# Optimization experiments

Measured on AMD Instinct MI355X. Metric: run time of the kernel, lower is better.

Reference implementation:

```python
import jax, jax.numpy as jnp
import numpy as np

M1, M2, BS = 2000, 400, 8
AT = M1 + M2
E1, E2, E3 = 60000, 20000, 20000
H, F, NG, L, C = 64, 64, 50, 4, 4
CUTOFF = 10.0
LOG2 = 0.6931471805599453  # shift of ShiftedSoftplus


def _ssp(x):
    return jax.nn.softplus(x) - LOG2


def _smear(d):
    # GaussianSmearing(0, cutoff, NG)
    offset = jnp.linspace(0.0, CUTOFF, NG)
    coeff = -0.5 / (offset[1] - offset[0]) ** 2
    return jnp.exp(coeff * (d[:, None] - offset[None, :]) ** 2)  # [E, NG]


def _colored_mlp(attr, colors, w1, b1, w2, b2):
    # w1:[C,NG,F] b1:[C,F] w2:[C,F,F] b2:[C,F]; route each edge through its color's MLP
    out = jnp.zeros((attr.shape[0], w1.shape[-1]), attr.dtype)
    for c in range(C):  # fixed small color count
        h = _ssp(attr @ w1[c] + b1[c]) @ w2[c] + b2[c]
        out = out + jnp.where((colors == c)[:, None], h, jnp.zeros((), attr.dtype))
    return out


def _block(h, ei, ew, attr, col, p):
    # InteractionBlock: CFConv -> ssp -> linear
    mw1, mb1, mw2, mb2, cw1, cw2, cb2, bw, bb = p
    Ccut = 0.5 * (jnp.cos(ew * jnp.pi / CUTOFF) + 1.0)
    W = _colored_mlp(attr, col, mw1, mb1, mw2, mb2) * Ccut[:, None]  # [E,F]
    x = h @ cw1                                   # lin1 (no bias) [N,F]
    msg = x[ei[:, 0]] * W                         # gather x_j, modulate
    agg = jax.ops.segment_sum(msg, ei[:, 1], num_segments=h.shape[0])  # scatter-add
    x = agg @ cw2 + cb2                           # lin2
    return _ssp(x) @ bw + bb                      # act + block linear


def _batch_graph(ei, ew, col):
    # replicate per-structure edges across the batch with node offset b*AT
    offs = (jnp.arange(BS, dtype=ei.dtype) * AT)[:, None, None]
    ei_b = (ei[None] + offs).reshape(-1, 2)
    return ei_b, jnp.tile(ew, BS), jnp.tile(col, BS)


def _forward(sites, sites_p, e1, ew1, c1, e2, ew2, c2, e3, ew3, c3,
             emb_w, emb_p_w, mlp_w1, mlp_b1, mlp_w2, mlp_b2,
             conv_w1, conv_w2, conv_b2, blk_w, blk_b,
             out_w1, out_b1, out_w2, out_b2):
    h = jnp.concatenate([emb_w[sites], emb_p_w[sites_p]], axis=1).reshape(BS * AT, H)
    graphs = []
    for (ei, ew, col) in ((e1, ew1, c1), (e2, ew2, c2), (e3, ew3, c3)):
        ei_b, ew_b, col_b = _batch_graph(ei, ew, col)
        graphs.append((ei_b, ew_b, col_b, _smear(ew_b)))
    for l in range(L):
        delta = jnp.zeros_like(h)
        for g, (ei_b, ew_b, col_b, attr_b) in enumerate(graphs):
            p = (mlp_w1[l, g], mlp_b1[l, g], mlp_w2[l, g], mlp_b2[l, g],
                 conv_w1[l, g], conv_w2[l, g], conv_b2[l, g], blk_w[l, g], blk_b[l, g])
            delta = delta + _block(h, ei_b, ew_b, attr_b, col_b, p)
        h = h + delta
    hp = h.reshape(BS, AT, H)[:, M1:, :]   # mask selects pore nodes only
    o = hp @ out_w1 + out_b1               # NB: original has `h - self.act(h)` no-op, so no activation here
    o = o @ out_w2 + out_b2                # [BS, M2, 1]
    return o.sum(axis=1)                   # 'add' readout per batch -> [BS, 1]


def setup_inputs() -> dict:
    key = jax.random.key(0)
    ks = jax.random.split(key, 24)
    f = lambda i, shape, s=0.1: jax.random.normal(ks[i], shape, jnp.float32) * s
    sites = jax.random.randint(ks[0], (BS, M1), 0, 1, dtype=jnp.int32)
    sites_p = jax.random.randint(ks[1], (BS, M2), 0, 2, dtype=jnp.int32)
    e1 = jax.random.randint(ks[2], (E1, 2), 0, M1, dtype=jnp.int32)
    e2 = jnp.stack([jax.random.randint(ks[3], (E2,), 0, M1, dtype=jnp.int32),
                    jax.random.randint(ks[4], (E2,), M1, AT, dtype=jnp.int32)], 1)
    e3 = jnp.stack([jax.random.randint(ks[5], (E3,), M1, AT, dtype=jnp.int32),
                    jax.random.randint(ks[6], (E3,), 0, M1, dtype=jnp.int32)], 1)
    ew1 = jax.random.uniform(ks[7], (E1,), jnp.float32, 0.5, CUTOFF)
    ew2 = jax.random.uniform(ks[8], (E2,), jnp.float32, 0.5, CUTOFF)
    ew3 = jax.random.uniform(ks[9], (E3,), jnp.float32, 0.5, CUTOFF)
    c1 = jax.random.randint(ks[10], (E1,), 0, C, dtype=jnp.int32)
    c2 = jax.random.randint(ks[11], (E2,), 0, C, dtype=jnp.int32)
    c3 = jax.random.randint(ks[12], (E3,), 0, C, dtype=jnp.int32)
    return {
        'sites': sites, 'sites_p': sites_p,
        'edge_idx1': e1, 'edge_weight1': ew1, 'colors1': c1,
        'edge_idx2': e2, 'edge_weight2': ew2, 'colors2': c2,
        'edge_idx3': e3, 'edge_weight3': ew3, 'colors3': c3,
        'emb_w': f(13, (1, H), 1.0), 'emb_p_w': f(14, (2, H), 1.0),
        'mlp_w1': f(15, (L, 3, C, NG, F)), 'mlp_b1': jnp.zeros((L, 3, C, F), jnp.float32),
        'mlp_w2': f(16, (L, 3, C, F, F)), 'mlp_b2': jnp.zeros((L, 3, C, F), jnp.float32),
        'conv_w1': f(17, (L, 3, H, F)), 'conv_w2': f(18, (L, 3, F, H)),
        'conv_b2': jnp.zeros((L, 3, H), jnp.float32),
        'blk_w': f(19, (L, 3, H, H)), 'blk_b': jnp.zeros((L, 3, H), jnp.float32),
        'out_w1': f(20, (H, H // 2)), 'out_b1': jnp.zeros((H // 2,), jnp.float32),
        'out_w2': f(21, (H // 2, 1)), 'out_b2': jnp.zeros((1,), jnp.float32),
    }


def reference(sites, sites_p, edge_idx1, edge_weight1, colors1,
              edge_idx2, edge_weight2, colors2, edge_idx3, edge_weight3, colors3,
              emb_w, emb_p_w, mlp_w1, mlp_b1, mlp_w2, mlp_b2,
              conv_w1, conv_w2, conv_b2, blk_w, blk_b,
              out_w1, out_b1, out_w2, out_b2):
    return _forward(sites, sites_p, edge_idx1, edge_weight1, colors1,
                    edge_idx2, edge_weight2, colors2, edge_idx3, edge_weight3, colors3,
                    emb_w, emb_p_w, mlp_w1, mlp_b1, mlp_w2, mlp_b2,
                    conv_w1, conv_w2, conv_b2, blk_w, blk_b,
                    out_w1, out_b1, out_w2, out_b2)
```

## Files before the change

kernel.cpp:

```cpp
#include <hip/hip_runtime.h>
#include <math.h>

constexpr int M1 = 2000, M2 = 400, BS = 8;
constexpr int AT = M1 + M2;
constexpr int NN = BS * AT;
constexpr int E1 = 60000, E2 = 20000, E3 = 20000;
constexpr int ET = E1 + E2 + E3;
constexpr int H = 64, F = 64, NG = 50, L = 4, C = 4;
constexpr float CUTOFF = 10.0f;
constexpr float LOG2F_ = 0.6931471805599453f;

constexpr float SMEAR_STEP = 10.0f / 49.0f;
constexpr float SMEAR_COEFF = -12.005f;
constexpr float PI_OVER_CUT = 0.31415926535897932f;

constexpr int NBLK = (ET + 255) / 256;

constexpr int NT = 512;
constexpr float DSCALE = (float)(NT - 1) / CUTOFF;

constexpr int TILE_M = 32;
constexpr int MT = NN / TILE_M;

constexpr int NB0 = M1 / 4;
constexpr int NB1 = M2 / 4;
constexpr int NB2 = M1 / 4;
constexpr int NBTOT = NB0 + NB1 + NB2;

constexpr size_t O_HA    = 0;
constexpr size_t O_HB    = O_HA  + (size_t)NN * 64 * 4;
constexpr size_t O_XG    = O_HB  + (size_t)NN * 64 * 4;
constexpr size_t O_DG    = O_XG  + (size_t)3 * AT * 512 * 2;
constexpr size_t O_TAB2  = O_DG  + (size_t)3 * NN * 64 * 4;
constexpr size_t O_EDATA = O_TAB2 + (size_t)48 * NT * 64 * 8;
constexpr size_t O_INT   = O_EDATA + (size_t)ET * 16;
constexpr int I_DEG  = 0;
constexpr int I_CUR  = 7200;
constexpr int I_ZEND = 14400;
constexpr int I_BASE = 14400;
constexpr int I_PERM = 21616;

__device__ inline float sspf(float x) {
    return fmaxf(x, 0.0f) + log1pf(expf(-fabsf(x))) - LOG2F_;
}
__device__ inline float sspf_fast(float x) {
    float t = __expf(-fabsf(x));
    return fmaxf(x, 0.0f) + __logf(1.0f + t) - LOG2F_;
}

__device__ inline unsigned short bf16rn(float x) {
    unsigned int u = __float_as_uint(x);
    u = (u + 0x7FFFu + ((u >> 16) & 1u)) >> 16;
    return (unsigned short)u;
}

__device__ inline int graph_off(int g) { return g == 0 ? 0 : (g == 1 ? E1 : E1 + E2); }

__device__ inline void edge_decode(int idx, int& g, int& e,
                                   const int* ei1, const int* ei2, const int* ei3,
                                   const int* c1, const int* c2, const int* c3,
                                   const int*& ei, const int*& cl) {
    if (idx < E1)            { g = 0; e = idx;           ei = ei1; cl = c1; }
    else if (idx < E1 + E2)  { g = 1; e = idx - E1;      ei = ei2; cl = c2; }
    else                     { g = 2; e = idx - E1 - E2; ei = ei3; cl = c3; }
}

__global__ void k_init_h(const int* __restrict__ sites, const int* __restrict__ sites_p,
                         const float* __restrict__ emb_w, const float* __restrict__ emb_p_w,
                         float* __restrict__ h) {
    int idx = blockIdx.x * blockDim.x + threadIdx.x;
    if (idx >= NN * 64) return;
    int f = idx & 63;
    int n = idx >> 6;
    int b = n / AT;
    int i = n - b * AT;
    float v;
    if (i < M1) v = emb_w[sites[b * M1 + i] * H + f];
    else        v = emb_p_w[sites_p[b * M2 + (i - M1)] * H + f];
    h[idx] = v;
}

__global__ void k_count(const int* __restrict__ ei1, const int* __restrict__ ei2,
                        const int* __restrict__ ei3, const int* __restrict__ c1,
                        const int* __restrict__ c2, const int* __restrict__ c3,
                        int* __restrict__ deg) {
    int idx = blockIdx.x * blockDim.x + threadIdx.x;
    if (idx >= ET) return;
    int g, e; const int* ei; const int* cl;
    edge_decode(idx, g, e, ei1, ei2, ei3, c1, c2, c3, ei, cl);
    atomicAdd(&deg[g * AT + ei[2 * e + 1]], 1);
}

__global__ void k_scan(const int* __restrict__ deg, int* __restrict__ base) {
    const int T = 256, CH = 10;
    int t = threadIdx.x;
    __shared__ int lsum[T];
    int g = blockIdx.x;
    int loc[CH];
    int s = 0;
    #pragma unroll
    for (int i = 0; i < CH; i++) {
        int idx = t * CH + i;
        int v = (idx < AT) ? deg[g * AT + idx] : 0;
        loc[i] = s;
        s += v;
    }
    lsum[t] = s;
    __syncthreads();
    for (int off = 1; off < T; off <<= 1) {
        int v = 0;
        if (t >= off) v = lsum[t - off];
        __syncthreads();
        lsum[t] += v;
        __syncthreads();
    }
    int tb = lsum[t] - s;
    #pragma unroll
    for (int i = 0; i < CH; i++) {
        int idx = t * CH + i;
        if (idx < AT) base[g * (AT + 1) + idx] = tb + loc[i];
    }
    if (t == T - 1) base[g * (AT + 1) + AT] = lsum[T - 1];
}

__global__ void k_sort(const int* __restrict__ deg, int* __restrict__ perm) {
    __shared__ int hist[256];
    __shared__ int cur[256];
    int g = blockIdx.x, t = threadIdx.x;
    int off   = (g == 1) ? M1 : 0;
    int cnt   = (g == 1) ? M2 : M1;
    int pbase = (g == 0) ? 0 : ((g == 1) ? M1 : (M1 + M2));
    hist[t] = 0;
    __syncthreads();
    for (int i = t; i < cnt; i += 256)
        atomicAdd(&hist[min(deg[g * AT + off + i], 255)], 1);
    __syncthreads();
    if (t == 0) {
        int run = 0;
        for (int k = 0; k < 256; k++) { cur[k] = run; run += hist[k]; }
    }
    __syncthreads();
    for (int i = t; i < cnt; i += 256) {
        int pos = atomicAdd(&cur[min(deg[g * AT + off + i], 255)], 1);
        perm[pbase + pos] = off + i;
    }
}

__global__ void k_fill(const int* __restrict__ ei1, const int* __restrict__ ei2,
                       const int* __restrict__ ei3, const int* __restrict__ c1,
                       const int* __restrict__ c2, const int* __restrict__ c3,
                       const float* __restrict__ ew1, const float* __restrict__ ew2,
                       const float* __restrict__ ew3,
                       const int* __restrict__ base, int* __restrict__ cur,
                       int4* __restrict__ edata) {
    int idx = blockIdx.x * blockDim.x + threadIdx.x;
    if (idx >= ET) return;
    int g, e; const int* ei; const int* cl;
    edge_decode(idx, g, e, ei1, ei2, ei3, c1, c2, c3, ei, cl);
    const float* ew = (g == 0) ? ew1 : (g == 1 ? ew2 : ew3);
    int dst = ei[2 * e + 1];
    int src = ei[2 * e];
    int p = base[g * (AT + 1) + dst] + atomicAdd(&cur[g * AT + dst], 1);
    float t = ew[e] * DSCALE;
    int i0 = min((int)t, NT - 2);
    float fr = t - (float)i0;
    int cb = cl[e] * (L * NT) + i0;
    edata[graph_off(g) + p] = make_int4(src, cb, __float_as_int(fr), 0);
}

__global__ __launch_bounds__(256) void k_table(
    const float* __restrict__ mlp_w1, const float* __restrict__ mlp_b1,
    const float* __restrict__ mlp_w2, const float* __restrict__ mlp_b2,
    float* __restrict__ tab2) {
    const int lane = threadIdx.x & 63;
    int w = blockIdx.x * 4 + (threadIdx.x >> 6);
    int s = w >> 9;
    int p = w & (NT - 1);
    int l = s % L;
    int gc = s / L;
    int c = gc % C;
    int g = gc / C;
    float d = (float)p * (CUTOFF / (float)(NT - 1));

    size_t wb = (size_t)((l * 3 + g) * C + c);
    const float* w1 = mlp_w1 + wb * NG * F;
    const float* w2 = mlp_w2 + wb * F * F;
    float w1c[NG], w2c[F];
    #pragma unroll
    for (int k = 0; k < NG; k++) w1c[k] = w1[k * F + lane];
    #pragma unroll
    for (int k = 0; k < F; k++) w2c[k] = w2[k * F + lane];
    float b1c = mlp_b1[wb * F + lane];
    float b2c = mlp_b2[wb * F + lane];

    float dd = d - (float)lane * SMEAR_STEP;
    float av = (lane < NG) ? __expf(SMEAR_COEFF * dd * dd) : 0.0f;
    float acc = b1c;
    #pragma unroll
    for (int k = 0; k < NG; k++) acc = fmaf(__shfl(av, k), w1c[k], acc);
    float t = sspf_fast(acc);
    float acc2 = b2c;
    #pragma unroll
    for (int j = 0; j < F; j++) acc2 = fmaf(__shfl(t, j), w2c[j], acc2);
    float ccut = 0.5f * (__cosf(d * PI_OVER_CUT) + 1.0f);
    float val = acc2 * ccut;
    tab2[((size_t)s * NT + p) * 128 + lane * 2] = val;
    if (p > 0)
        tab2[((size_t)s * NT + (p - 1)) * 128 + lane * 2 + 1] = val;
}

__device__ inline void fma4(float acc[4], float a, const float4 b) {
    acc[0] = fmaf(a, b.x, acc[0]);
    acc[1] = fmaf(a, b.y, acc[1]);
    acc[2] = fmaf(a, b.z, acc[2]);
    acc[3] = fmaf(a, b.w, acc[3]);
}

__device__ inline void stage_A(const float* __restrict__ gA, float (*As)[68], int t) {
    #pragma unroll
    for (int i = 0; i < 2; i++) {
        int v = t + i * 256;
        int r = v >> 4, c4 = (v & 15) * 4;
        *(float4*)&As[r][c4] = *(const float4*)(gA + (size_t)r * 64 + c4);
    }
}
__device__ inline void stage_B(const float* __restrict__ gB, float (*Bs)[68], int t) {
    #pragma unroll
    for (int i = 0; i < 4; i++) {
        int v = t + i * 256;
        int r = v >> 4, c4 = (v & 15) * 4;
        *(float4*)&Bs[r][c4] = *(const float4*)(gB + (size_t)r * 64 + c4);
    }
}
__device__ inline void gemm_tile(const float (*As)[68], const float (*Bs)[68],
                                 int r0, int c0, float acc0[4], float acc1[4]) {
    #pragma unroll 4
    for (int k0 = 0; k0 < 64; k0 += 4) {
        float4 a0 = *(const float4*)&As[r0][k0];
        float4 a1 = *(const float4*)&As[r0 + 1][k0];
        float4 b0 = *(const float4*)&Bs[k0][c0];
        float4 b1 = *(const float4*)&Bs[k0 + 1][c0];
        float4 b2 = *(const float4*)&Bs[k0 + 2][c0];
        float4 b3 = *(const float4*)&Bs[k0 + 3][c0];
        fma4(acc0, a0.x, b0); fma4(acc0, a0.y, b1);
        fma4(acc0, a0.z, b2); fma4(acc0, a0.w, b3);
        fma4(acc1, a1.x, b0); fma4(acc1, a1.y, b1);
        fma4(acc1, a1.z, b2); fma4(acc1, a1.w, b3);
    }
}

__device__ inline void store_xg(unsigned short* __restrict__ xg, int g, int n,
                                int c0, const float acc[4]) {
    int b = n / AT;
    int i = n - b * AT;
    unsigned short* out = xg + (((size_t)g * AT + i) * 8 + b) * 64 + c0;
    ushort4 v;
    v.x = bf16rn(acc[0]);
    v.y = bf16rn(acc[1]);
    v.z = bf16rn(acc[2]);
    v.w = bf16rn(acc[3]);
    *(ushort4*)out = v;
}

__global__ __launch_bounds__(256) void k_lin1t(
    const float* __restrict__ h, const float* __restrict__ conv_w1,
    unsigned short* __restrict__ xg, int l) {
    __shared__ float As[TILE_M][68];
    __shared__ float Bs[64][68];
    int t = threadIdx.x;
    int g = blockIdx.x / MT;
    int tile = blockIdx.x - g * MT;
    stage_A(h + (size_t)tile * TILE_M * 64, As, t);
    stage_B(conv_w1 + (size_t)(l * 3 + g) * 64 * 64, Bs, t);
    __syncthreads();
    int cg = t & 15, rg = t >> 4;
    int c0 = cg * 4, r0 = rg * 2;
    float acc0[4] = {0, 0, 0, 0}, acc1[4] = {0, 0, 0, 0};
    gemm_tile(As, Bs, r0, c0, acc0, acc1);
    int n0 = tile * TILE_M;
    store_xg(xg, g, n0 + r0, c0, acc0);
    store_xg(xg, g, n0 + r0 + 1, c0, acc1);
}

__device__ inline void acc_edge_bf(float acc[8], float wl, const uint4 q, int c0) {
    acc[0] = fmaf(__uint_as_float(q.x << 16),         __shfl(wl, c0 + 0), acc[0]);
    acc[1] = fmaf(__uint_as_float(q.x & 0xFFFF0000u), __shfl(wl, c0 + 1), acc[1]);
    acc[2] = fmaf(__uint_as_float(q.y << 16),         __shfl(wl, c0 + 2), acc[2]);
    acc[3] = fmaf(__uint_as_float(q.y & 0xFFFF0000u), __shfl(wl, c0 + 3), acc[3]);
    acc[4] = fmaf(__uint_as_float(q.z << 16),         __shfl(wl, c0 + 4), acc[4]);
    acc[5] = fmaf(__uint_as_float(q.z & 0xFFFF0000u), __shfl(wl, c0 + 5), acc[5]);
    acc[6] = fmaf(__uint_as_float(q.w << 16),         __shfl(wl, c0 + 6), acc[6]);
    acc[7] = fmaf(__uint_as_float(q.w & 0xFFFF0000u), __shfl(wl, c0 + 7), acc[7]);
}

__global__ __launch_bounds__(256) void k_aggl(
    const int4* __restrict__ edata, const int* __restrict__ base,
    const int* __restrict__ perm,
    const unsigned short* __restrict__ xg, const float* __restrict__ tab2,
    const float* __restrict__ conv_w2, const float* __restrict__ conv_b2,
    const float* __restrict__ blk_w, const float* __restrict__ blk_b,
    float* __restrict__ dg, int l) {
    __shared__ float As[TILE_M][68];
    __shared__ float Bs[64][68];
    int t = threadIdx.x;
    const int lane = t & 63;
    const int wv = t >> 6;
    int bid = blockIdx.x;
    int g, grp, nbg, pbase;
    if (bid < NB0)            { g = 0; grp = bid;             nbg = NB0; pbase = 0; }
    else if (bid < NB0 + NB1) { g = 1; grp = bid - NB0;       nbg = NB1; pbase = M1; }
    else                      { g = 2; grp = bid - NB0 - NB1; nbg = NB2; pbase = M1 + M2; }
    int gi = nbg - 1 - grp;
    int dst = perm[pbase + gi * 4 + wv];
    size_t pb = (size_t)(l * 3 + g);
    stage_B(conv_w2 + pb * 4096, Bs, t);

    const int b = lane >> 3;
    const int c0 = (lane & 7) * 8;
    const int4* ed = edata + graph_off(g);
    int s = base[g * (AT + 1) + dst];
    int e = base[g * (AT + 1) + dst + 1];
    const float2* tg = (const float2*)tab2 +
                       ((size_t)g * C * L * NT + (size_t)l * NT) * 64;
    const unsigned short* xgg = xg + (size_t)g * AT * 512;
    float acc[8];
    #pragma unroll
    for (int j = 0; j < 8; j++) acc[j] = 0.0f;

    int i = s;
    while (i < e) {
        int cnt = min(e - i, 64);
        int4 mrec = ed[i + min(lane, cnt - 1)];
        int j = 0;
        for (; j + 4 <= cnt; j += 4) {
            int x0 = __shfl(mrec.x, j),     y0 = __shfl(mrec.y, j),     z0 = __shfl(mrec.z, j);
            int x1 = __shfl(mrec.x, j + 1), y1 = __shfl(mrec.y, j + 1), z1 = __shfl(mrec.z, j + 1);
            int x2 = __shfl(mrec.x, j + 2), y2 = __shfl(mrec.y, j + 2), z2 = __shfl(mrec.z, j + 2);
            int x3 = __shfl(mrec.x, j + 3), y3 = __shfl(mrec.y, j + 3), z3 = __shfl(mrec.z, j + 3);
            float2 rv0 = tg[(size_t)y0 * 64 + lane];
            float2 rv1 = tg[(size_t)y1 * 64 + lane];
            float2 rv2 = tg[(size_t)y2 * 64 + lane];
            float2 rv3 = tg[(size_t)y3 * 64 + lane];
            uint4 q0 = *(const uint4*)(xgg + ((size_t)x0 * 8 + b) * 64 + c0);
            uint4 q1 = *(const uint4*)(xgg + ((size_t)x1 * 8 + b) * 64 + c0);
            uint4 q2 = *(const uint4*)(xgg + ((size_t)x2 * 8 + b) * 64 + c0);
            uint4 q3 = *(const uint4*)(xgg + ((size_t)x3 * 8 + b) * 64 + c0);
            float wl0 = fmaf(__int_as_float(z0), rv0.y - rv0.x, rv0.x);
            float wl1 = fmaf(__int_as_float(z1), rv1.y - rv1.x, rv1.x);
            float wl2 = fmaf(__int_as_float(z2), rv2.y - rv2.x, rv2.x);
            float wl3 = fmaf(__int_as_float(z3), rv3.y - rv3.x, rv3.x);
            acc_edge_bf(acc, wl0, q0, c0);
            acc_edge_bf(acc, wl1, q1, c0);
            acc_edge_bf(acc, wl2, q2, c0);
            acc_edge_bf(acc, wl3, q3, c0);
        }
        for (; j < cnt; j++) {
            int x0 = __shfl(mrec.x, j), y0 = __shfl(mrec.y, j), z0 = __shfl(mrec.z, j);
            float2 rv = tg[(size_t)y0 * 64 + lane];
            float wl = fmaf(__int_as_float(z0), rv.y - rv.x, rv.x);
            uint4 q = *(const uint4*)(xgg + ((size_t)x0 * 8 + b) * 64 + c0);
            acc_edge_bf(acc, wl, q, c0);
        }
        i += cnt;
    }
    *(float4*)&As[wv * 8 + b][c0]     = make_float4(acc[0], acc[1], acc[2], acc[3]);
    *(float4*)&As[wv * 8 + b][c0 + 4] = make_float4(acc[4], acc[5], acc[6], acc[7]);
    __syncthreads();

    int cg = t & 15, rg = t >> 4;
    int cc0 = cg * 4, r0 = rg * 2;
    float4 bias = *(const float4*)(conv_b2 + pb * 64 + cc0);
    float a0[4] = {bias.x, bias.y, bias.z, bias.w};
    float a1[4] = {bias.x, bias.y, bias.z, bias.w};
    gemm_tile(As, Bs, r0, cc0, a0, a1);
    __syncthreads();
    *(float4*)&As[r0][cc0] =
        make_float4(sspf(a0[0]), sspf(a0[1]), sspf(a0[2]), sspf(a0[3]));
    *(float4*)&As[r0 + 1][cc0] =
        make_float4(sspf(a1[0]), sspf(a1[1]), sspf(a1[2]), sspf(a1[3]));
    stage_B(blk_w + pb * 4096, Bs, t);
    __syncthreads();
    float4 bb = *(const float4*)(blk_b + pb * 64 + cc0);
    float b0[4] = {bb.x, bb.y, bb.z, bb.w};
    float b1[4] = {bb.x, bb.y, bb.z, bb.w};
    gemm_tile(As, Bs, r0, cc0, b0, b1);
    int dstR = perm[pbase + gi * 4 + (r0 >> 3)];
    float* dp0 = dg + ((size_t)g * NN + (size_t)(r0 & 7) * AT + dstR) * 64 + cc0;
    float* dp1 = dg + ((size_t)g * NN + (size_t)((r0 + 1) & 7) * AT + dstR) * 64 + cc0;
    *(float4*)dp0 = make_float4(b0[0], b0[1], b0[2], b0[3]);
    *(float4*)dp1 = make_float4(b1[0], b1[1], b1[2], b1[3]);
}

__global__ __launch_bounds__(256) void k_lin1f(
    const float* __restrict__ hIn, float* __restrict__ hOut,
    const float* __restrict__ dg, const float* __restrict__ conv_w1,
    const float* __restrict__ conv_b2, const float* __restrict__ blk_w,
    const float* __restrict__ blk_b,
    unsigned short* __restrict__ xg, int lcur, int last) {
    __shared__ float As[TILE_M][68];
    __shared__ float Bs[64][68];
    __shared__ float cv[3][64];
    int t = threadIdx.x;
    int g, tile;
    if (last) { g = 0; tile = blockIdx.x; }
    else      { g = blockIdx.x / MT; tile = blockIdx.x - g * MT; }
    int wvi = t >> 6, lane = t & 63;
    if (wvi < 3) {
        size_t pbg = (size_t)(lcur * 3 + wvi);
        float sl = sspf(conv_b2[pbg * 64 + lane]);
        const float* bw = blk_w + pbg * 4096;
        float a = blk_b[pbg * 64 + lane];
        #pragma unroll 8
        for (int k = 0; k < 64; k++)
            a = fmaf(__shfl(sl, k), bw[k * 64 + lane], a);
        cv[wvi][lane] = a;
    }
    __syncthreads();
    size_t off = (size_t)tile * TILE_M * 64;
    int n0 = tile * TILE_M;
    int bb_ = n0 / AT;
    int i0 = n0 - bb_ * AT;
    #pragma unroll
    for (int i = 0; i < 2; i++) {
        int v = t + i * 256;
        int r = v >> 4, c4 = (v & 15) * 4;
        size_t o = off + (size_t)r * 64 + c4;
        float4 hv = *(const float4*)(hIn + o);
        int node_i = i0 + r;
        if (node_i < M1) {
            float4 d0 = *(const float4*)(dg + o);
            float4 d2 = *(const float4*)(dg + (size_t)2 * NN * 64 + o);
            float4 c1v = *(const float4*)&cv[1][c4];
            hv.x += d0.x + c1v.x + d2.x;
            hv.y += d0.y + c1v.y + d2.y;
            hv.z += d0.z + c1v.z + d2.z;
            hv.w += d0.w + c1v.w + d2.w;
        } else {
            float4 d1 = *(const float4*)(dg + (size_t)NN * 64 + o);
            float4 c0v = *(const float4*)&cv[0][c4];
            float4 c2v = *(const float4*)&cv[2][c4];
            hv.x += c0v.x + d1.x + c2v.x;
            hv.y += c0v.y + d1.y + c2v.y;
            hv.z += c0v.z + d1.z + c2v.z;
            hv.w += c0v.w + d1.w + c2v.w;
        }
        *(float4*)&As[r][c4] = hv;
        if (g == 0) *(float4*)(hOut + o) = hv;
    }
    if (last) return;
    stage_B(conv_w1 + (size_t)((lcur + 1) * 3 + g) * 4096, Bs, t);
    __syncthreads();
    int cg = t & 15, rg = t >> 4;
    int c0 = cg * 4, r0 = rg * 2;
    float acc0[4] = {0, 0, 0, 0}, acc1[4] = {0, 0, 0, 0};
    gemm_tile(As, Bs, r0, c0, acc0, acc1);
    store_xg(xg, g, n0 + r0, c0, acc0);
    store_xg(xg, g, n0 + r0 + 1, c0, acc1);
}

__global__ void k_read(const float* __restrict__ h,
                       const float* __restrict__ w1, const float* __restrict__ b1,
                       const float* __restrict__ w2, const float* __restrict__ b2,
                       float* __restrict__ out) {
    int b = blockIdx.x;
    int lane = threadIdx.x & 63;
    int wv = threadIdx.x >> 6;
    __shared__ float part[4];
    float weff = 0.0f;
    #pragma unroll
    for (int j = 0; j < H / 2; j++) weff = fmaf(w1[lane * (H / 2) + j], w2[j], weff);
    float acc = 0.0f;
    for (int i = wv * (M2 / 4); i < (wv + 1) * (M2 / 4); i++)
        acc += h[((size_t)b * AT + M1 + i) * H + lane];
    float v = acc * weff;
    for (int off = 32; off; off >>= 1) v += __shfl_xor(v, off);
    if (lane == 0) part[wv] = v;
    __syncthreads();
    if (threadIdx.x == 0) {
        float bias = b2[0];
        for (int j = 0; j < H / 2; j++) bias = fmaf(b1[j], w2[j], bias);
        out[b] = part[0] + part[1] + part[2] + part[3] + (float)M2 * bias;
    }
}

extern "C" void kernel_launch(void* const* d_in, const int* in_sizes, int n_in,
                              void* d_out, int out_size, void* d_ws, size_t ws_size,
                              hipStream_t stream) {
    const int* sites   = (const int*)d_in[0];
    const int* sites_p = (const int*)d_in[1];
    const int* ei1 = (const int*)d_in[2];
    const float* ew1 = (const float*)d_in[3];
    const int* c1 = (const int*)d_in[4];
    const int* ei2 = (const int*)d_in[5];
    const float* ew2 = (const float*)d_in[6];
    const int* c2 = (const int*)d_in[7];
    const int* ei3 = (const int*)d_in[8];
    const float* ew3 = (const float*)d_in[9];
    const int* c3 = (const int*)d_in[10];
    const float* emb_w   = (const float*)d_in[11];
    const float* emb_p_w = (const float*)d_in[12];
    const float* mlp_w1 = (const float*)d_in[13];
    const float* mlp_b1 = (const float*)d_in[14];
    const float* mlp_w2 = (const float*)d_in[15];
    const float* mlp_b2 = (const float*)d_in[16];
    const float* conv_w1 = (const float*)d_in[17];
    const float* conv_w2 = (const float*)d_in[18];
    const float* conv_b2 = (const float*)d_in[19];
    const float* blk_w = (const float*)d_in[20];
    const float* blk_b = (const float*)d_in[21];
    const float* out_w1 = (const float*)d_in[22];
    const float* out_b1 = (const float*)d_in[23];
    const float* out_w2 = (const float*)d_in[24];
    const float* out_b2 = (const float*)d_in[25];

    char* ws = (char*)d_ws;
    float* hA   = (float*)(ws + O_HA);
    float* hB   = (float*)(ws + O_HB);
    unsigned short* xg = (unsigned short*)(ws + O_XG);
    float* dg   = (float*)(ws + O_DG);
    float* tab2 = (float*)(ws + O_TAB2);
    int4*  edata = (int4*)(ws + O_EDATA);
    int* ip    = (int*)(ws + O_INT);
    int* deg   = ip + I_DEG;
    int* cur   = ip + I_CUR;
    int* ibase = ip + I_BASE;
    int* dperm = ip + I_PERM;

    hipMemsetAsync(ip, 0, (size_t)I_ZEND * sizeof(int), stream);

    k_table<<<48 * NT / 4, 256, 0, stream>>>(mlp_w1, mlp_b1, mlp_w2, mlp_b2, tab2);
    k_init_h<<<(NN * 64 + 255) / 256, 256, 0, stream>>>(sites, sites_p, emb_w, emb_p_w, hA);
    k_count<<<NBLK, 256, 0, stream>>>(ei1, ei2, ei3, c1, c2, c3, deg);
    k_scan<<<3, 256, 0, stream>>>(deg, ibase);
    k_sort<<<3, 256, 0, stream>>>(deg, dperm);
    k_fill<<<NBLK, 256, 0, stream>>>(ei1, ei2, ei3, c1, c2, c3, ew1, ew2, ew3,
                                     ibase, cur, edata);

    k_lin1t<<<3 * MT, 256, 0, stream>>>(hA, conv_w1, xg, 0);
    float* hcur = hA;
    float* hnxt = hB;
    for (int l = 0; l < L; l++) {
        int last = (l == L - 1) ? 1 : 0;
        k_aggl<<<NBTOT, 256, 0, stream>>>(edata, ibase, dperm, xg, tab2,
                                          conv_w2, conv_b2, blk_w, blk_b,
                                          dg, l);
        k_lin1f<<<last ? MT : 3 * MT, 256, 0, stream>>>(hcur, hnxt, dg, conv_w1,
                                                        conv_b2, blk_w, blk_b,
                                                        xg, l, last);
        float* tmp = hcur; hcur = hnxt; hnxt = tmp;
    }
    k_read<<<BS, 256, 0, stream>>>(hcur, out_w1, out_b1, out_w2, out_b2, (float*)d_out);
}
```

Measured before the change: 391.7 us.

## Transpose xg layout to channel-major batch-packed bf16 to drop shuffles in aggregation

Changes the bf16 xg buffer from [node][batch][channel] to [node][channel][batch], so each lane in the aggregation kernel owns one channel across all 8 batch copies. This removes the per-edge __shfl of the edge weight for each channel: every lane uses its own interpolated weight directly. To produce the new layout, lin1 kernels now gather rows batch-interleaved per node group, stage the GEMM result through shared memory with extra barriers, and write packed uint4 words. The aggregation edge loop is also unrolled by 2 instead of 4, which lowers register pressure but exposes less memory-level parallelism.

```diff
diff --git a/kernel.cpp b/kernel.cpp
--- a/kernel.cpp
+++ b/kernel.cpp
@@ -48,10 +48,10 @@
     return fmaxf(x, 0.0f) + __logf(1.0f + t) - LOG2F_;
 }
 
-__device__ inline unsigned short bf16rn(float x) {
+__device__ inline unsigned int bf16rn(float x) {
     unsigned int u = __float_as_uint(x);
     u = (u + 0x7FFFu + ((u >> 16) & 1u)) >> 16;
-    return (unsigned short)u;
+    return u & 0xFFFFu;
 }
 
 __device__ inline int graph_off(int g) { return g == 0 ? 0 : (g == 1 ? E1 : E1 + E2); }
@@ -216,14 +216,6 @@
     acc[3] = fmaf(a, b.w, acc[3]);
 }
 
-__device__ inline void stage_A(const float* __restrict__ gA, float (*As)[68], int t) {
-    #pragma unroll
-    for (int i = 0; i < 2; i++) {
-        int v = t + i * 256;
-        int r = v >> 4, c4 = (v & 15) * 4;
-        *(float4*)&As[r][c4] = *(const float4*)(gA + (size_t)r * 64 + c4);
-    }
-}
 __device__ inline void stage_B(const float* __restrict__ gB, float (*Bs)[68], int t) {
     #pragma unroll
     for (int i = 0; i < 4; i++) {
@@ -249,17 +241,16 @@
     }
 }
 
-__device__ inline void store_xg(unsigned short* __restrict__ xg, int g, int n,
-                                int c0, const float acc[4]) {
-    int b = n / AT;
-    int i = n - b * AT;
-    unsigned short* out = xg + (((size_t)g * AT + i) * 8 + b) * 64 + c0;
-    ushort4 v;
-    v.x = bf16rn(acc[0]);
-    v.y = bf16rn(acc[1]);
-    v.z = bf16rn(acc[2]);
-    v.w = bf16rn(acc[3]);
-    *(ushort4*)out = v;
+__device__ inline void xg_transpose_store(const float (*T)[68],
+                                          unsigned short* __restrict__ xg,
+                                          int g, int i0, int t) {
+    int k = t >> 6, c = t & 63;
+    unsigned int w0 = bf16rn(T[k * 8 + 0][c]) | (bf16rn(T[k * 8 + 1][c]) << 16);
+    unsigned int w1 = bf16rn(T[k * 8 + 2][c]) | (bf16rn(T[k * 8 + 3][c]) << 16);
+    unsigned int w2 = bf16rn(T[k * 8 + 4][c]) | (bf16rn(T[k * 8 + 5][c]) << 16);
+    unsigned int w3 = bf16rn(T[k * 8 + 6][c]) | (bf16rn(T[k * 8 + 7][c]) << 16);
+    unsigned short* out = xg + (((size_t)g * AT + i0 + k) * 64 + c) * 8;
+    *(uint4*)out = make_uint4(w0, w1, w2, w3);
 }
 
 __global__ __launch_bounds__(256) void k_lin1t(
@@ -269,28 +260,26 @@
     __shared__ float Bs[64][68];
     int t = threadIdx.x;
     int g = blockIdx.x / MT;
-    int tile = blockIdx.x - g * MT;
-    stage_A(h + (size_t)tile * TILE_M * 64, As, t);
-    stage_B(conv_w1 + (size_t)(l * 3 + g) * 64 * 64, Bs, t);
+    int igrp = blockIdx.x - g * MT;
+    int i0 = igrp * 4;
+    #pragma unroll
+    for (int it = 0; it < 2; it++) {
+        int v = t + it * 256;
+        int r = v >> 4, c4 = (v & 15) * 4;
+        int n = (r & 7) * AT + i0 + (r >> 3);
+        *(float4*)&As[r][c4] = *(const float4*)(h + (size_t)n * 64 + c4);
+    }
+    stage_B(conv_w1 + (size_t)(l * 3 + g) * 4096, Bs, t);
     __syncthreads();
     int cg = t & 15, rg = t >> 4;
     int c0 = cg * 4, r0 = rg * 2;
     float acc0[4] = {0, 0, 0, 0}, acc1[4] = {0, 0, 0, 0};
     gemm_tile(As, Bs, r0, c0, acc0, acc1);
-    int n0 = tile * TILE_M;
-    store_xg(xg, g, n0 + r0, c0, acc0);
-    store_xg(xg, g, n0 + r0 + 1, c0, acc1);
-}
-
-__device__ inline void acc_edge_bf(float acc[8], float wl, const uint4 q, int c0) {
-    acc[0] = fmaf(__uint_as_float(q.x << 16),         __shfl(wl, c0 + 0), acc[0]);
-    acc[1] = fmaf(__uint_as_float(q.x & 0xFFFF0000u), __shfl(wl, c0 + 1), acc[1]);
-    acc[2] = fmaf(__uint_as_float(q.y << 16),         __shfl(wl, c0 + 2), acc[2]);
-    acc[3] = fmaf(__uint_as_float(q.y & 0xFFFF0000u), __shfl(wl, c0 + 3), acc[3]);
-    acc[4] = fmaf(__uint_as_float(q.z << 16),         __shfl(wl, c0 + 4), acc[4]);
-    acc[5] = fmaf(__uint_as_float(q.z & 0xFFFF0000u), __shfl(wl, c0 + 5), acc[5]);
-    acc[6] = fmaf(__uint_as_float(q.w << 16),         __shfl(wl, c0 + 6), acc[6]);
-    acc[7] = fmaf(__uint_as_float(q.w & 0xFFFF0000u), __shfl(wl, c0 + 7), acc[7]);
+    __syncthreads();
+    *(float4*)&As[r0][c0]     = make_float4(acc0[0], acc0[1], acc0[2], acc0[3]);
+    *(float4*)&As[r0 + 1][c0] = make_float4(acc1[0], acc1[1], acc1[2], acc1[3]);
+    __syncthreads();
+    xg_transpose_store(As, xg, g, i0, t);
 }
 
 __global__ __launch_bounds__(256) void k_aggl(
@@ -315,8 +304,6 @@
     size_t pb = (size_t)(l * 3 + g);
     stage_B(conv_w2 + pb * 4096, Bs, t);
 
-    const int b = lane >> 3;
-    const int c0 = (lane & 7) * 8;
     const int4* ed = edata + graph_off(g);
     int s = base[g * (AT + 1) + dst];
     int e = base[g * (AT + 1) + dst + 1];
@@ -332,39 +319,50 @@
         int cnt = min(e - i, 64);
         int4 mrec = ed[i + min(lane, cnt - 1)];
         int j = 0;
-        for (; j + 4 <= cnt; j += 4) {
+        for (; j + 2 <= cnt; j += 2) {
             int x0 = __shfl(mrec.x, j),     y0 = __shfl(mrec.y, j),     z0 = __shfl(mrec.z, j);
             int x1 = __shfl(mrec.x, j + 1), y1 = __shfl(mrec.y, j + 1), z1 = __shfl(mrec.z, j + 1);
-            int x2 = __shfl(mrec.x, j + 2), y2 = __shfl(mrec.y, j + 2), z2 = __shfl(mrec.z, j + 2);
-            int x3 = __shfl(mrec.x, j + 3), y3 = __shfl(mrec.y, j + 3), z3 = __shfl(mrec.z, j + 3);
             float2 rv0 = tg[(size_t)y0 * 64 + lane];
             float2 rv1 = tg[(size_t)y1 * 64 + lane];
-            float2 rv2 = tg[(size_t)y2 * 64 + lane];
-            float2 rv3 = tg[(size_t)y3 * 64 + lane];
-            uint4 q0 = *(const uint4*)(xgg + ((size_t)x0 * 8 + b) * 64 + c0);
-            uint4 q1 = *(const uint4*)(xgg + ((size_t)x1 * 8 + b) * 64 + c0);
-            uint4 q2 = *(const uint4*)(xgg + ((size_t)x2 * 8 + b) * 64 + c0);
-            uint4 q3 = *(const uint4*)(xgg + ((size_t)x3 * 8 + b) * 64 + c0);
+            uint4 q0 = *(const uint4*)(xgg + ((size_t)x0 * 64 + lane) * 8);
+            uint4 q1 = *(const uint4*)(xgg + ((size_t)x1 * 64 + lane) * 8);
             float wl0 = fmaf(__int_as_float(z0), rv0.y - rv0.x, rv0.x);
             float wl1 = fmaf(__int_as_float(z1), rv1.y - rv1.x, rv1.x);
-            float wl2 = fmaf(__int_as_float(z2), rv2.y - rv2.x, rv2.x);
-            float wl3 = fmaf(__int_as_float(z3), rv3.y - rv3.x, rv3.x);
-            acc_edge_bf(acc, wl0, q0, c0);
-            acc_edge_bf(acc, wl1, q1, c0);
-            acc_edge_bf(acc, wl2, q2, c0);
-            acc_edge_bf(acc, wl3, q3, c0);
+            acc[0] = fmaf(__uint_as_float(q0.x << 16),         wl0, acc[0]);
+            acc[1] = fmaf(__uint_as_float(q0.x & 0xFFFF0000u), wl0, acc[1]);
+            acc[2] = fmaf(__uint_as_float(q0.y << 16),         wl0, acc[2]);
+            acc[3] = fmaf(__uint_as_float(q0.y & 0xFFFF0000u), wl0, acc[3]);
+            acc[4] = fmaf(__uint_as_float(q0.z << 16),         wl0, acc[4]);
+            acc[5] = fmaf(__uint_as_float(q0.z & 0xFFFF0000u), wl0, acc[5]);
+            acc[6] = fmaf(__uint_as_float(q0.w << 16),         wl0, acc[6]);
+            acc[7] = fmaf(__uint_as_float(q0.w & 0xFFFF0000u), wl0, acc[7]);
+            acc[0] = fmaf(__uint_as_float(q1.x << 16),         wl1, acc[0]);
+            acc[1] = fmaf(__uint_as_float(q1.x & 0xFFFF0000u), wl1, acc[1]);
+            acc[2] = fmaf(__uint_as_float(q1.y << 16),         wl1, acc[2]);
+            acc[3] = fmaf(__uint_as_float(q1.y & 0xFFFF0000u), wl1, acc[3]);
+            acc[4] = fmaf(__uint_as_float(q1.z << 16),         wl1, acc[4]);
+            acc[5] = fmaf(__uint_as_float(q1.z & 0xFFFF0000u), wl1, acc[5]);
+            acc[6] = fmaf(__uint_as_float(q1.w << 16),         wl1, acc[6]);
+            acc[7] = fmaf(__uint_as_float(q1.w & 0xFFFF0000u), wl1, acc[7]);
         }
-        for (; j < cnt; j++) {
+        if (j < cnt) {
             int x0 = __shfl(mrec.x, j), y0 = __shfl(mrec.y, j), z0 = __shfl(mrec.z, j);
             float2 rv = tg[(size_t)y0 * 64 + lane];
             float wl = fmaf(__int_as_float(z0), rv.y - rv.x, rv.x);
-            uint4 q = *(const uint4*)(xgg + ((size_t)x0 * 8 + b) * 64 + c0);
-            acc_edge_bf(acc, wl, q, c0);
+            uint4 q = *(const uint4*)(xgg + ((size_t)x0 * 64 + lane) * 8);
+            acc[0] = fmaf(__uint_as_float(q.x << 16),         wl, acc[0]);
+            acc[1] = fmaf(__uint_as_float(q.x & 0xFFFF0000u), wl, acc[1]);
+            acc[2] = fmaf(__uint_as_float(q.y << 16),         wl, acc[2]);
+            acc[3] = fmaf(__uint_as_float(q.y & 0xFFFF0000u), wl, acc[3]);
+            acc[4] = fmaf(__uint_as_float(q.z << 16),         wl, acc[4]);
+            acc[5] = fmaf(__uint_as_float(q.z & 0xFFFF0000u), wl, acc[5]);
+            acc[6] = fmaf(__uint_as_float(q.w << 16),         wl, acc[6]);
+            acc[7] = fmaf(__uint_as_float(q.w & 0xFFFF0000u), wl, acc[7]);
         }
         i += cnt;
     }
-    *(float4*)&As[wv * 8 + b][c0]     = make_float4(acc[0], acc[1], acc[2], acc[3]);
-    *(float4*)&As[wv * 8 + b][c0 + 4] = make_float4(acc[4], acc[5], acc[6], acc[7]);
+    #pragma unroll
+    for (int b2 = 0; b2 < 8; b2++) As[wv * 8 + b2][lane] = acc[b2];
     __syncthreads();
 
     int cg = t & 15, rg = t >> 4;
@@ -401,9 +399,10 @@
     __shared__ float Bs[64][68];
     __shared__ float cv[3][64];
     int t = threadIdx.x;
-    int g, tile;
-    if (last) { g = 0; tile = blockIdx.x; }
-    else      { g = blockIdx.x / MT; tile = blockIdx.x - g * MT; }
+    int g, igrp;
+    if (last) { g = 0; igrp = blockIdx.x; }
+    else      { g = blockIdx.x / MT; igrp = blockIdx.x - g * MT; }
+    int i0 = igrp * 4;
     int wvi = t >> 6, lane = t & 63;
     if (wvi < 3) {
         size_t pbg = (size_t)(lcur * 3 + wvi);
@@ -416,17 +415,14 @@
         cv[wvi][lane] = a;
     }
     __syncthreads();
-    size_t off = (size_t)tile * TILE_M * 64;
-    int n0 = tile * TILE_M;
-    int bb_ = n0 / AT;
-    int i0 = n0 - bb_ * AT;
-    #pragma unroll
-    for (int i = 0; i < 2; i++) {
-        int v = t + i * 256;
+    #pragma unroll
+    for (int it = 0; it < 2; it++) {
+        int v = t + it * 256;
         int r = v >> 4, c4 = (v & 15) * 4;
-        size_t o = off + (size_t)r * 64 + c4;
+        int k = r >> 3, b = r & 7;
+        int node_i = i0 + k;
+        size_t o = ((size_t)b * AT + node_i) * 64 + c4;
         float4 hv = *(const float4*)(hIn + o);
-        int node_i = i0 + r;
         if (node_i < M1) {
             float4 d0 = *(const float4*)(dg + o);
             float4 d2 = *(const float4*)(dg + (size_t)2 * NN * 64 + o);
@@ -454,8 +450,11 @@
     int c0 = cg * 4, r0 = rg * 2;
     float acc0[4] = {0, 0, 0, 0}, acc1[4] = {0, 0, 0, 0};
     gemm_tile(As, Bs, r0, c0, acc0, acc1);
-    store_xg(xg, g, n0 + r0, c0, acc0);
-    store_xg(xg, g, n0 + r0 + 1, c0, acc1);
+    __syncthreads();
+    *(float4*)&As[r0][c0]     = make_float4(acc0[0], acc0[1], acc0[2], acc0[3]);
+    *(float4*)&As[r0 + 1][c0] = make_float4(acc1[0], acc1[1], acc1[2], acc1[3]);
+    __syncthreads();
+    xg_transpose_store(As, xg, g, i0, t);
 }
 
 __global__ void k_read(const float* __restrict__ h,
```

Result: faster. 365.1 us (-6.8%).
